# Optimization experiments

Hardware: AMD Instinct MI355X
Metric: run time of the kernel (lower is better)

## Reference

```python
import jax, jax.numpy as jnp
import numpy as np

S = 64.0
MARGIN = 0.5

def setup_inputs() -> dict:
    key = jax.random.key(0)
    k1, k2 = jax.random.split(key)
    B, C = 256, 100000
    # cosine similarities in (-0.99, 0.99) so arccos is well-conditioned
    logits = jax.random.uniform(k1, (B, C), dtype=jnp.float32, minval=-0.99, maxval=0.99)
    labels = jax.random.randint(k2, (B,), 0, C, dtype=jnp.int64)
    return {"logits": logits, "labels": labels}

def _arcface(logits, labels):
    B = logits.shape[0]
    valid = labels != -1                     # rows with a real target
    safe_labels = jnp.where(valid, labels, 0)
    rows = jnp.arange(B)
    target = logits[rows, safe_labels]       # [B] target cosines
    # original does arccos over the whole matrix then cos back; off-target
    # entries reduce to identity, targets become cos(arccos(x) + m)
    new_target = jnp.cos(jnp.arccos(target) + MARGIN)
    new_target = jnp.where(valid, new_target, target)
    modified = logits.at[rows, safe_labels].set(new_target)
    # the no_grad block + custom Function make backward exactly grad * s
    return S * (logits + jax.lax.stop_gradient(modified - logits))

def reference(logits, labels):
    return _arcface(logits, labels)
```

## Files before the change

### kernel.cpp

```cpp
#include <hip/hip_runtime.h>
#include <hip/hip_bf16.h>
#include <math.h>


#define ARC_S      64.0f
#define COS_M      0.8775825618903728f
#define SIN_M      0.4794255386042030f

typedef float floatx4 __attribute__((ext_vector_type(4)));

__global__ __launch_bounds__(256) void scale_copy_kernel(
    const floatx4* __restrict__ in,
    floatx4*       __restrict__ out)
{
    const size_t base = (size_t)blockIdx.x * 2048u + threadIdx.x;

    floatx4 v[8];
    #pragma unroll
    for (int j = 0; j < 8; ++j)
        v[j] = in[base + j * 256];

    #pragma unroll
    for (int j = 0; j < 8; ++j) {
        floatx4 w = v[j] * ARC_S;
        __builtin_nontemporal_store(w, &out[base + j * 256]);
    }
}

__global__ __launch_bounds__(256) void fixup_kernel(
    const float* __restrict__ logits,
    const int*   __restrict__ labels,
    float*       __restrict__ out,
    int B, int C, size_t tailStart, size_t total)
{
    const int t = threadIdx.x;

    if (t < B) {
        const int lbl = labels[t];
        if (lbl >= 0 && lbl < C) {
            const size_t idx = (size_t)t * (size_t)C + (size_t)lbl;
            const float x = logits[idx];
            const float s = sqrtf(fmaxf(0.0f, 1.0f - x * x));
            out[idx] = ARC_S * (x * COS_M - s * SIN_M);
        }
    }

    for (size_t i = tailStart + t; i < total; i += 256)
        out[i] = ARC_S * logits[i];
}

extern "C" void kernel_launch(void* const* d_in, const int* in_sizes, int n_in,
                              void* d_out, int out_size, void* d_ws, size_t ws_size,
                              hipStream_t stream) {
    const float* logits = (const float*)d_in[0];
    const int*   labels = (const int*)d_in[1];
    float*       out    = (float*)d_out;

    const int B = in_sizes[1];
    const int C = in_sizes[0] / B;
    const size_t total  = (size_t)B * (size_t)C;
    const size_t total4 = total / 4;
    const int    nChunks = (int)(total4 / 2048);
    const size_t tailStart = (size_t)nChunks * 2048u * 4u;

    scale_copy_kernel<<<dim3(nChunks), dim3(256), 0, stream>>>(
        (const floatx4*)logits, (floatx4*)out);
    fixup_kernel<<<dim3(1), dim3(256), 0, stream>>>(
        logits, labels, out, B, C, tailStart, total);
}
```

Before: 180.8 us.

## Use persistent grid-stride copy with inline-asm loads and regular stores

Replaces the one-block-per-chunk launch with a grid capped at 2048 blocks that loops over chunks. It issues the eight vector loads through inline assembly ending in a full wait, and uses ordinary stores in place of nontemporal ones. The aim is to cut block launch overhead and control how the loads are issued. The cost is that the explicit full wait stops loads from overlapping across iterations, and the normal stores may pollute the cache.

```diff
diff --git a/kernel.cpp b/kernel.cpp
--- a/kernel.cpp
+++ b/kernel.cpp
@@ -11,19 +11,38 @@
 
 __global__ __launch_bounds__(256) void scale_copy_kernel(
     const floatx4* __restrict__ in,
-    floatx4*       __restrict__ out)
+    floatx4*       __restrict__ out,
+    int nUnits)
 {
-    const size_t base = (size_t)blockIdx.x * 2048u + threadIdx.x;
+    const int t = threadIdx.x;
+    for (int bu = blockIdx.x; bu < nUnits; bu += gridDim.x) {
+        const size_t base = (size_t)bu * 2048u + (size_t)t;
+        const floatx4* p = in + base;
 
-    floatx4 v[8];
-    #pragma unroll
-    for (int j = 0; j < 8; ++j)
-        v[j] = in[base + j * 256];
+        floatx4 v0, v1, v2, v3, v4, v5, v6, v7;
+        asm volatile(
+            "global_load_dwordx4 %0, %8, off\n\t"
+            "global_load_dwordx4 %1, %9, off\n\t"
+            "global_load_dwordx4 %2, %10, off\n\t"
+            "global_load_dwordx4 %3, %11, off\n\t"
+            "global_load_dwordx4 %4, %12, off\n\t"
+            "global_load_dwordx4 %5, %13, off\n\t"
+            "global_load_dwordx4 %6, %14, off\n\t"
+            "global_load_dwordx4 %7, %15, off\n\t"
+            "s_waitcnt vmcnt(0)"
+            : "=&v"(v0), "=&v"(v1), "=&v"(v2), "=&v"(v3),
+              "=&v"(v4), "=&v"(v5), "=&v"(v6), "=&v"(v7)
+            : "v"(p),        "v"(p + 256),  "v"(p + 512),  "v"(p + 768),
+              "v"(p + 1024), "v"(p + 1280), "v"(p + 1536), "v"(p + 1792));
 
-    #pragma unroll
-    for (int j = 0; j < 8; ++j) {
-        floatx4 w = v[j] * ARC_S;
-        __builtin_nontemporal_store(w, &out[base + j * 256]);
+        out[base         ] = v0 * ARC_S;
+        out[base +  256u ] = v1 * ARC_S;
+        out[base +  512u ] = v2 * ARC_S;
+        out[base +  768u ] = v3 * ARC_S;
+        out[base + 1024u ] = v4 * ARC_S;
+        out[base + 1280u ] = v5 * ARC_S;
+        out[base + 1536u ] = v6 * ARC_S;
+        out[base + 1792u ] = v7 * ARC_S;
     }
 }
 
@@ -60,11 +79,13 @@
     const int C = in_sizes[0] / B;
     const size_t total  = (size_t)B * (size_t)C;
     const size_t total4 = total / 4;
-    const int    nChunks = (int)(total4 / 2048);
-    const size_t tailStart = (size_t)nChunks * 2048u * 4u;
+    const int    nUnits = (int)(total4 / 2048);
+    const size_t tailStart = (size_t)nUnits * 2048u * 4u;
 
-    scale_copy_kernel<<<dim3(nChunks), dim3(256), 0, stream>>>(
-        (const floatx4*)logits, (floatx4*)out);
+    const int nBlocks = nUnits < 2048 ? nUnits : 2048;
+
+    scale_copy_kernel<<<dim3(nBlocks), dim3(256), 0, stream>>>(
+        (const floatx4*)logits, (floatx4*)out, nUnits);
     fixup_kernel<<<dim3(1), dim3(256), 0, stream>>>(
         logits, labels, out, B, C, tailStart, total);
 }
```

New measurement: 186.3 us. 1.03x slower.
